# Kernel tuning notes

Hardware: AMD Instinct MI355X
Metric: run time of the kernel (lower is better)

The kernel has to match this reference:

```python
import math
import jax, jax.numpy as jnp
import numpy as np

NL, D, FF, V, S, BS, H = 6, 256, 1024, 1024, 48, 64, 8
NUM_CONT, NUM_CAT = 32, 16
TEMP = 0.1

def _pos_enc(L, d):
    pos = jnp.arange(L, dtype=jnp.float32)[:, None]
    div = jnp.exp(jnp.arange(0, d, 2, dtype=jnp.float32) * (-math.log(10000.0) / d))
    pe = jnp.zeros((L, d), jnp.float32)
    pe = pe.at[:, 0::2].set(jnp.sin(pos * div))
    pe = pe.at[:, 1::2].set(jnp.cos(pos * div))
    return pe

def _ln(x, w, b, eps=1e-5):
    m = x.mean(-1, keepdims=True)
    v = ((x - m) ** 2).mean(-1, keepdims=True)
    return (x - m) * jax.lax.rsqrt(v + eps) * w + b

def _mha(q_in, kv_in, wqkv, bqkv, wo, bo, mask=None):
    d = q_in.shape[-1]; dh = d // H
    wq, wk, wv = jnp.split(wqkv, 3, axis=0)
    bq, bk, bv = jnp.split(bqkv, 3)
    def proj(x, w, b):
        y = x @ w.T + b
        return y.reshape(x.shape[0], x.shape[1], H, dh).transpose(0, 2, 1, 3)
    q, k, v = proj(q_in, wq, bq), proj(kv_in, wk, bk), proj(kv_in, wv, bv)
    s = jnp.einsum('bhqd,bhkd->bhqk', q, k) * (1.0 / math.sqrt(dh))
    if mask is not None:
        s = s + mask
    a = jax.nn.softmax(s, axis=-1)
    o = jnp.einsum('bhqk,bhkd->bhqd', a, v).transpose(0, 2, 1, 3).reshape(q_in.shape)
    return o @ wo.T + bo

def setup_inputs() -> dict:
    key = jax.random.key(0)
    ks = iter(jax.random.split(key, 64))
    g = lambda shape: jax.random.normal(next(ks), shape, jnp.float32) * 0.02
    return dict(
        x_cont=jax.random.randint(next(ks), (BS, NUM_CONT), 0, V),
        x_cat=jax.random.randint(next(ks), (BS, NUM_CAT), 0, V),
        sos=g((1, 1, D)),
        emb_tab=g((S, V, D)),            # stacked per-feature embedding tables
        head_w=g((S, V, D)), head_b=jnp.zeros((S, V)),
        enc_wqkv=g((NL, 3 * D, D)), enc_bqkv=jnp.zeros((NL, 3 * D)),
        enc_wo=g((NL, D, D)), enc_bo=jnp.zeros((NL, D)),
        enc_w1=g((NL, FF, D)), enc_b1=jnp.zeros((NL, FF)),
        enc_w2=g((NL, D, FF)), enc_b2=jnp.zeros((NL, D)),
        enc_lnw=jnp.ones((NL, 2, D)), enc_lnb=jnp.zeros((NL, 2, D)),
        dec_swqkv=g((NL, 3 * D, D)), dec_sbqkv=jnp.zeros((NL, 3 * D)),
        dec_swo=g((NL, D, D)), dec_sbo=jnp.zeros((NL, D)),
        dec_cwqkv=g((NL, 3 * D, D)), dec_cbqkv=jnp.zeros((NL, 3 * D)),
        dec_cwo=g((NL, D, D)), dec_cbo=jnp.zeros((NL, D)),
        dec_w1=g((NL, FF, D)), dec_b1=jnp.zeros((NL, FF)),
        dec_w2=g((NL, D, FF)), dec_b2=jnp.zeros((NL, D)),
        dec_lnw=jnp.ones((NL, 3, D)), dec_lnb=jnp.zeros((NL, 3, D)),
        lnf_w=jnp.ones((2, D)), lnf_b=jnp.zeros((2, D)),
    )

def reference(x_cont, x_cat, sos, emb_tab, head_w, head_b,
              enc_wqkv, enc_bqkv, enc_wo, enc_bo, enc_w1, enc_b1, enc_w2, enc_b2,
              enc_lnw, enc_lnb,
              dec_swqkv, dec_sbqkv, dec_swo, dec_sbo,
              dec_cwqkv, dec_cbqkv, dec_cwo, dec_cbo,
              dec_w1, dec_b1, dec_w2, dec_b2, dec_lnw, dec_lnb, lnf_w, lnf_b):
    bs = x_cont.shape[0]
    pe = _pos_enc(S + 1, D)
    # ---- encoder over the 48 source features (post-norm, ReLU) ----
    idx = jnp.concatenate([x_cont, x_cat], axis=1)            # [bs, S]
    x = emb_tab[jnp.arange(S)[None, :], idx] + pe[None, :S]   # [bs, S, D]
    for l in range(NL):
        a = _mha(x, x, enc_wqkv[l], enc_bqkv[l], enc_wo[l], enc_bo[l])
        x = _ln(x + a, enc_lnw[l, 0], enc_lnb[l, 0])
        f = jax.nn.relu(x @ enc_w1[l].T + enc_b1[l]) @ enc_w2[l].T + enc_b2[l]
        x = _ln(x + f, enc_lnw[l, 1], enc_lnb[l, 1])
    memory = _ln(x, lnf_w[0], lnf_b[0])

    Lt = S + 1
    causal = jnp.triu(jnp.full((Lt, Lt), -1e9, jnp.float32), k=1)

    def decode(tgt):  # full decoder stack recomputed every step (no KV cache)
        y = tgt
        for l in range(NL):
            a = _mha(y, y, dec_swqkv[l], dec_sbqkv[l], dec_swo[l], dec_sbo[l], causal)
            y = _ln(y + a, dec_lnw[l, 0], dec_lnb[l, 0])
            c = _mha(y, memory, dec_cwqkv[l], dec_cbqkv[l], dec_cwo[l], dec_cbo[l])
            y = _ln(y + c, dec_lnw[l, 1], dec_lnb[l, 1])
            f = jax.nn.relu(y @ dec_w1[l].T + dec_b1[l]) @ dec_w2[l].T + dec_b2[l]
            y = _ln(y + f, dec_lnw[l, 2], dec_lnb[l, 2])
        return _ln(y, lnf_w[1], lnf_b[1])

    buf0 = jnp.zeros((bs, Lt, D), jnp.float32).at[:, 0].set(sos[0, 0])
    step_keys = jax.random.split(jax.random.key(42), S)

    def step(buf, xs):
        i, k, hw, hb, et = xs
        h = decode(buf + pe[None])          # [bs, Lt, D]
        hi = jnp.take(h, i, axis=1)          # last generated position [bs, D]
        logits = hi @ hw.T + hb              # [bs, V]
        choice = jax.random.categorical(k, logits / TEMP)
        buf = buf.at[:, i + 1].set(et[choice])
        return buf, (choice, logits)

    _, (choices, logits_all) = jax.lax.scan(
        step, buf0, (jnp.arange(S), step_keys, head_w, head_b, emb_tab))
    s_cont = choices[:NUM_CONT].T            # [bs, num_cont]
    s_cat = choices[NUM_CONT:].T             # [bs, num_cat]
    return s_cont, s_cat, logits_all
```

## Files before the change

kernel.cpp:

```cpp
#include <hip/hip_runtime.h>
#include <math.h>

#define JAX_PARTITIONABLE 1


static constexpr int SWQKVT  = 0;
static constexpr int SWOT    = SWQKVT + 6*256*768;
static constexpr int CWQT    = SWOT   + 6*256*256;
static constexpr int CWOT    = CWQT   + 6*256*256;
static constexpr int DW1T    = CWOT   + 6*256*256;
static constexpr int DW2T    = DW1T   + 6*256*1024;
static constexpr int WT_END  = DW2T   + 6*1024*256;
static constexpr int CKT_OFF = WT_END;
static constexpr int CV_OFF  = CKT_OFF + 6*64*48*256;
static constexpr int SKT_OFF = CV_OFF  + 6*64*48*256;
static constexpr int SV_OFF  = SKT_OFF + 6*64*48*256;
static constexpr int WS_END  = SV_OFF  + 6*64*48*256;
static constexpr int X_OFF    = 0;
static constexpr int MEM_OFF  = X_OFF + 3072*256;
static constexpr int QKV_OFF  = SKT_OFF;
static constexpr int AO_OFF   = QKV_OFF + 3072*768;
static constexpr int RES1_OFF = AO_OFF + 3072*256;
static constexpr int X1_OFF   = RES1_OFF + 3072*256;
static constexpr int HB_OFF   = SV_OFF;
static constexpr int RES2_OFF = HB_OFF + 3072*1024;
static constexpr int PCK_OFF  = SKT_OFF;

struct GParams {
  const int   *xc, *xct;
  const float *sos, *emb, *hw, *hb;
  const float *ewqkv, *ebqkv, *ewo, *ebo, *ew1, *eb1, *ew2, *eb2, *elnw, *elnb;
  const float *swqkv, *sbqkv, *swo, *sbo;
  const float *cwqkv, *cbqkv, *cwo, *cbo;
  const float *dw1, *db1, *dw2, *db2, *dlnw, *dlnb, *lnfw, *lnfb;
  float *out;
  float *ws;
};

__device__ unsigned g_cntA = 0, g_genA = 0;

static __device__ __forceinline__ void gbar(unsigned* cnt, unsigned* gen, unsigned nb) {
  __syncthreads();
  if (threadIdx.x == 0) {
    __threadfence();
    unsigned g = __hip_atomic_load(gen, __ATOMIC_RELAXED, __HIP_MEMORY_SCOPE_AGENT);
    unsigned prev = __hip_atomic_fetch_add(cnt, 1u, __ATOMIC_ACQ_REL, __HIP_MEMORY_SCOPE_AGENT);
    if (prev == nb - 1u) {
      __hip_atomic_store(cnt, 0u, __ATOMIC_RELAXED, __HIP_MEMORY_SCOPE_AGENT);
      __threadfence();
      __hip_atomic_store(gen, g + 1u, __ATOMIC_RELEASE, __HIP_MEMORY_SCOPE_AGENT);
    } else {
      while (__hip_atomic_load(gen, __ATOMIC_ACQUIRE, __HIP_MEMORY_SCOPE_AGENT) == g)
        __builtin_amdgcn_s_sleep(1);
      __threadfence();
    }
  }
  __syncthreads();
}

static __device__ __forceinline__ void tf2x32(unsigned k0, unsigned k1, unsigned& x0, unsigned& x1) {
  unsigned ks2 = k0 ^ k1 ^ 0x1BD11BDAu;
  x0 += k0; x1 += k1;
#define TF_R(r) { x0 += x1; x1 = (x1 << r) | (x1 >> (32 - r)); x1 ^= x0; }
  TF_R(13) TF_R(15) TF_R(26) TF_R(6)   x0 += k1;  x1 += ks2 + 1u;
  TF_R(17) TF_R(29) TF_R(16) TF_R(24)  x0 += ks2; x1 += k0  + 2u;
  TF_R(13) TF_R(15) TF_R(26) TF_R(6)   x0 += k0;  x1 += k1  + 3u;
  TF_R(17) TF_R(29) TF_R(16) TF_R(24)  x0 += k1;  x1 += ks2 + 4u;
  TF_R(13) TF_R(15) TF_R(26) TF_R(6)   x0 += ks2; x1 += k0  + 5u;
#undef TF_R
}

static __device__ __forceinline__ void step_key(int i, unsigned& k0, unsigned& k1) {
#if JAX_PARTITIONABLE
  unsigned x0 = 0u, x1 = (unsigned)i;
  tf2x32(0u, 42u, x0, x1);
  k0 = x0; k1 = x1;
#else
  unsigned w[2];
  for (int wi = 0; wi < 2; wi++) {
    unsigned o = (unsigned)(2*i + wi), x0, x1;
    if (o < 48u) { x0 = o; x1 = 48u + o; tf2x32(0u, 42u, x0, x1); w[wi] = x0; }
    else         { x0 = o - 48u; x1 = o; tf2x32(0u, 42u, x0, x1); w[wi] = x1; }
  }
  k0 = w[0]; k1 = w[1];
#endif
}

static __device__ __forceinline__ unsigned gumbel_bits(unsigned k0, unsigned k1, int b, int v) {
#if JAX_PARTITIONABLE
  unsigned x0 = 0u, x1 = (unsigned)(b*1024 + v);
  tf2x32(k0, k1, x0, x1);
  return x0 ^ x1;
#else
  unsigned jj = (unsigned)((b & 31)*1024 + v);
  unsigned x0 = jj, x1 = 32768u + jj;
  tf2x32(k0, k1, x0, x1);
  return (b < 32) ? x0 : x1;
#endif
}

static __device__ __forceinline__ float pe_val(int p, int c) {
  const float KC = (float)(-9.210340371976184 / 256.0);
  int j = c >> 1;
  float dv = expf((float)(2*j) * KC);
  float a = (float)p * dv;
  return (c & 1) ? cosf(a) : sinf(a);
}

static __device__ __forceinline__ void wave_ln_row(float* row, const float* lw, const float* lb) {
  const int lane = threadIdx.x & 63;
  float x0 = row[lane], x1 = row[lane+64], x2 = row[lane+128], x3 = row[lane+192];
  float s = (x0 + x1) + (x2 + x3);
#pragma unroll
  for (int m = 1; m < 64; m <<= 1) s += __shfl_xor(s, m);
  float mean = s * 0.00390625f;
  float d0 = x0-mean, d1 = x1-mean, d2 = x2-mean, d3 = x3-mean;
  float q = (d0*d0 + d1*d1) + (d2*d2 + d3*d3);
#pragma unroll
  for (int m = 1; m < 64; m <<= 1) q += __shfl_xor(q, m);
  float rs = 1.0f / sqrtf(q * 0.00390625f + 1e-5f);
  row[lane]     = d0*rs*lw[lane]     + lb[lane];
  row[lane+64]  = d1*rs*lw[lane+64]  + lb[lane+64];
  row[lane+128] = d2*rs*lw[lane+128] + lb[lane+128];
  row[lane+192] = d3*rs*lw[lane+192] + lb[lane+192];
}

template<int C, int KS, int K>
static __device__ void matvec_t(const float* __restrict__ wt, const float* __restrict__ x,
                                float* __restrict__ part) {
  const int t = threadIdx.x;
  constexpr int O4 = C/4;
  constexpr int KC = K/KS;
  if (t < O4*KS) {
    const int kc = t / O4, o4 = t - kc*O4;
    const int k0 = kc*KC;
    float4 acc = {0.f,0.f,0.f,0.f};
    const float* wp = wt + k0*C + o4*4;
    for (int kb = 0; kb < KC; kb += 16) {
      float4 w[16];
#pragma unroll
      for (int j = 0; j < 16; j++) w[j] = *(const float4*)(wp + (kb + j)*C);
#pragma unroll
      for (int j4 = 0; j4 < 4; j4++) {
        float4 xv = *(const float4*)(x + k0 + kb + j4*4);
        float4 a0 = w[j4*4+0], a1 = w[j4*4+1], a2 = w[j4*4+2], a3 = w[j4*4+3];
        acc.x += xv.x*a0.x; acc.y += xv.x*a0.y; acc.z += xv.x*a0.z; acc.w += xv.x*a0.w;
        acc.x += xv.y*a1.x; acc.y += xv.y*a1.y; acc.z += xv.y*a1.z; acc.w += xv.y*a1.w;
        acc.x += xv.z*a2.x; acc.y += xv.z*a2.y; acc.z += xv.z*a2.z; acc.w += xv.z*a2.w;
        acc.x += xv.w*a3.x; acc.y += xv.w*a3.y; acc.z += xv.w*a3.z; acc.w += xv.w*a3.w;
      }
    }
    *(float4*)(part + kc*C + o4*4) = acc;
  }
  __syncthreads();
}

static __device__ void gemm_stage(const float* __restrict__ A, const float* __restrict__ W,
                                  const float* __restrict__ bias, const float* __restrict__ res,
                                  float* __restrict__ out, int R, int C, int K, int relu,
                                  float* sA) {
  const int t = threadIdx.x;
  const bool act = (t < 256);
  const int lane = t & 63, wv = (t >> 6) & 3;
  const int ntc = C >> 6;
  const int ntiles = (R >> 5) * ntc;
  for (int tile = blockIdx.x; tile < ntiles; tile += gridDim.x) {
    const int tr = tile / ntc, tc = tile - tr*ntc;
    const int r0 = tr << 5;
    const int c  = (tc << 6) + lane;
    float acc[8] = {0,0,0,0,0,0,0,0};
    for (int kc = 0; kc < K; kc += 256) {
      __syncthreads();
      if (act) {
#pragma unroll
        for (int u = 0; u < 8; u++) {
          int idx = u*256 + t;
          int rr = idx >> 6, cc = idx & 63;
          ((float4*)sA)[idx] = *(const float4*)(A + (r0+rr)*K + kc + cc*4);
        }
      }
      __syncthreads();
      if (act) {
        const float* wr = W + c*K + kc;
        for (int k = 0; k < 256; k += 4) {
          float4 w4 = *(const float4*)(wr + k);
#pragma unroll
          for (int r = 0; r < 8; r++) {
            float4 a4 = *(const float4*)(sA + (wv*8 + r)*256 + k);
            acc[r] += a4.x*w4.x; acc[r] += a4.y*w4.y; acc[r] += a4.z*w4.z; acc[r] += a4.w*w4.w;
          }
        }
      }
    }
    if (act) {
      float bb = bias ? bias[c] : 0.0f;
#pragma unroll
      for (int r = 0; r < 8; r++) {
        int row = r0 + wv*8 + r;
        float v = acc[r] + bb;
        if (relu) v = fmaxf(v, 0.0f);
        if (res)  v += res[row*C + c];
        out[row*C + c] = v;
      }
    }
  }
}

static __device__ void ln_stage(const float* in, const float* lw, const float* lb,
                                float* out, int R) {
  const int lane = threadIdx.x & 63;
  int gw = blockIdx.x*8 + (threadIdx.x >> 6);
  for (int row = gw; row < R; row += gridDim.x*8) {
    const float* ir = in + row*256;
    float x0 = ir[lane], x1 = ir[lane+64], x2 = ir[lane+128], x3 = ir[lane+192];
    float s = (x0 + x1) + (x2 + x3);
#pragma unroll
    for (int m = 1; m < 64; m <<= 1) s += __shfl_xor(s, m);
    float mean = s * 0.00390625f;
    float d0 = x0-mean, d1 = x1-mean, d2 = x2-mean, d3 = x3-mean;
    float q = (d0*d0 + d1*d1) + (d2*d2 + d3*d3);
#pragma unroll
    for (int m = 1; m < 64; m <<= 1) q += __shfl_xor(q, m);
    float rs = 1.0f / sqrtf(q * 0.00390625f + 1e-5f);
    float* orow = out + row*256;
    orow[lane]     = d0*rs*lw[lane]     + lb[lane];
    orow[lane+64]  = d1*rs*lw[lane+64]  + lb[lane+64];
    orow[lane+128] = d2*rs*lw[lane+128] + lb[lane+128];
    orow[lane+192] = d3*rs*lw[lane+192] + lb[lane+192];
  }
}

static __device__ void attn_core(const float* qd, const float* kb, const float* vb,
                                 int krstride, int kstride, int nk,
                                 float* sc, float* red, float* ao) {
  const int t = threadIdx.x;
  const int r = t >> 5, p0 = t & 31;
  const bool act = (t < 256);
  if (act) {
#pragma unroll
    for (int pass = 0; pass < 2; pass++) {
      int p = pass*32 + p0;
      if (p < nk) {
        const float4* k4 = (const float4*)(kb + r*krstride + p*kstride);
        const float4* q4 = (const float4*)(qd + r*32);
        float a = 0.0f;
#pragma unroll
        for (int d4 = 0; d4 < 8; d4++) {
          float4 kv = k4[d4], qv = q4[d4];
          a += qv.x*kv.x; a += qv.y*kv.y; a += qv.z*kv.z; a += qv.w*kv.w;
        }
        sc[r*48 + p] = a * 0.17677669529663687f;
      }
    }
  }
  __syncthreads();
  if (t < 8) {
    float m = sc[t*48];
    for (int p = 1; p < nk; p++) m = fmaxf(m, sc[t*48 + p]);
    red[t] = m;
  }
  __syncthreads();
  if (act) {
#pragma unroll
    for (int pass = 0; pass < 2; pass++) {
      int p = pass*32 + p0;
      if (p < nk) sc[r*48 + p] = expf(sc[r*48 + p] - red[r]);
    }
  }
  __syncthreads();
  if (t < 8) {
    float s = 0.0f;
    for (int p = 0; p < nk; p++) s += sc[t*48 + p];
    red[8 + t] = s;
  }
  __syncthreads();
  if (act) {
#pragma unroll
    for (int pass = 0; pass < 2; pass++) {
      int p = pass*32 + p0;
      if (p < nk) sc[r*48 + p] = sc[r*48 + p] / red[8 + r];
    }
  }
  __syncthreads();
  if (act) {
    const int d2 = t & 31;
    const float* vr = vb + r*krstride + d2;
    float a = 0.0f;
    for (int p = 0; p < nk; p++) a += sc[r*48 + p] * vr[p*kstride];
    ao[r*32 + d2] = a;
  }
  __syncthreads();
}

static __device__ void enc_attn_stage(const float* QKV, float* AO, float* sm) {
  const int t = threadIdx.x;
  const bool act = (t < 256);
  float* qd  = sm;
  float* sc  = sm + 256;
  float* ao  = sm + 640;
  float* red = sm + 896;
  for (int pi = blockIdx.x; pi < 512; pi += gridDim.x) {
    int b = pi >> 3, h = pi & 7;
    const float* Qb = QKV + b*48*768 + h*32;
    const float* Kb = QKV + b*48*768 + 256 + h*32;
    const float* Vb = QKV + b*48*768 + 512 + h*32;
    for (int qg = 0; qg < 6; qg++) {
      if (act) { int r = t >> 5, d2 = t & 31; qd[r*32 + d2] = Qb[(qg*8 + r)*768 + d2]; }
      __syncthreads();
      attn_core(qd, Kb, Vb, 0, 768, 48, sc, red, ao);
      if (act) { int r = t >> 5, d2 = t & 31; AO[(b*48 + qg*8 + r)*256 + h*32 + d2] = ao[r*32 + d2]; }
      __syncthreads();
    }
  }
}

static __device__ void attn_dec(const float* qd, const float* kt, const float* v,
                                int nk, float* sc, float* red, float* ao) {
  const int t = threadIdx.x;
  const int r = t >> 5, p0 = t & 31;
  const bool act = (t < 256);
  if (act) {
    const float4* q4 = (const float4*)(qd + r*32);
#pragma unroll
    for (int pass = 0; pass < 2; pass++) {
      int p = pass*32 + p0;
      if (p < nk) {
        const float* kb = kt + r*1536 + p*4;
        float a = 0.0f;
#pragma unroll
        for (int j = 0; j < 8; j++) {
          float4 kv = *(const float4*)(kb + j*192);
          float4 qv = q4[j];
          a += qv.x*kv.x; a += qv.y*kv.y; a += qv.z*kv.z; a += qv.w*kv.w;
        }
        sc[r*48 + p] = a * 0.17677669529663687f;
      }
    }
  }
  __syncthreads();
  if (t < 8) {
    float m = sc[t*48];
    for (int p = 1; p < nk; p++) m = fmaxf(m, sc[t*48 + p]);
    red[t] = m;
  }
  __syncthreads();
  if (act) {
#pragma unroll
    for (int pass = 0; pass < 2; pass++) {
      int p = pass*32 + p0;
      if (p < nk) sc[r*48 + p] = expf(sc[r*48 + p] - red[r]);
    }
  }
  __syncthreads();
  if (t < 8) {
    float s = 0.0f;
    for (int p = 0; p < nk; p++) s += sc[t*48 + p];
    red[8 + t] = s;
  }
  __syncthreads();
  if (act) {
#pragma unroll
    for (int pass = 0; pass < 2; pass++) {
      int p = pass*32 + p0;
      if (p < nk) sc[r*48 + p] = sc[r*48 + p] / red[8 + r];
    }
  }
  __syncthreads();
  if (act) {
    const int d2 = t & 31;
    const float* vr = v + r*32 + d2;
    float a = 0.0f;
    int p = 0;
    for (; p + 8 <= nk; p += 8) {
      float vv[8], ss[8];
#pragma unroll
      for (int j = 0; j < 8; j++) { vv[j] = vr[(p+j)*256]; ss[j] = sc[r*48 + p + j]; }
#pragma unroll
      for (int j = 0; j < 8; j++) a += ss[j] * vv[j];
    }
    for (; p < nk; p++) a += sc[r*48 + p] * vr[p*256];
    ao[r*32 + d2] = a;
  }
  __syncthreads();
}

__global__ void __launch_bounds__(512)
genrev5_kernel(GParams P) {
  __shared__ float sm[8448];
  float* ws = P.ws;
  const int wg = blockIdx.x;
  const int t  = threadIdx.x;

  if (t < 256) {
    for (int rr = 0; rr < 12; rr++) {
      int row = wg*12 + rr;
      int b = row / 48, s = row % 48;
      int tok = (s < 32) ? P.xc[b*32 + s] : P.xct[b*16 + (s - 32)];
      ws[X_OFF + row*256 + t] = P.emb[(s*1024 + tok)*256 + t] + pe_val(s, t);
    }
  }
  gbar(&g_cntA, &g_genA, 256);

  float* Xp = ws + X_OFF;
  for (int l = 0; l < 6; l++) {
    gemm_stage(Xp, P.ewqkv + l*768*256, P.ebqkv + l*768, nullptr, ws + QKV_OFF, 3072, 768, 256, 0, sm);
    gbar(&g_cntA, &g_genA, 256);
    enc_attn_stage(ws + QKV_OFF, ws + AO_OFF, sm);
    gbar(&g_cntA, &g_genA, 256);
    gemm_stage(ws + AO_OFF, P.ewo + l*256*256, P.ebo + l*256, Xp, ws + RES1_OFF, 3072, 256, 256, 0, sm);
    gbar(&g_cntA, &g_genA, 256);
    ln_stage(ws + RES1_OFF, P.elnw + (l*2 + 0)*256, P.elnb + (l*2 + 0)*256, ws + X1_OFF, 3072);
    gbar(&g_cntA, &g_genA, 256);
    gemm_stage(ws + X1_OFF, P.ew1 + l*1024*256, P.eb1 + l*1024, nullptr, ws + HB_OFF, 3072, 1024, 256, 1, sm);
    gbar(&g_cntA, &g_genA, 256);
    gemm_stage(ws + HB_OFF, P.ew2 + l*256*1024, P.eb2 + l*256, ws + X1_OFF, ws + RES2_OFF, 3072, 256, 1024, 0, sm);
    gbar(&g_cntA, &g_genA, 256);
    ln_stage(ws + RES2_OFF, P.elnw + (l*2 + 1)*256, P.elnb + (l*2 + 1)*256, Xp, 3072);
    gbar(&g_cntA, &g_genA, 256);
  }
  ln_stage(Xp, P.lnfw, P.lnfb, ws + MEM_OFF, 3072);
  gbar(&g_cntA, &g_genA, 256);
  for (int l = 0; l < 6; l++) {
    gemm_stage(ws + MEM_OFF, P.cwqkv + (l*768 + 256)*256, P.cbqkv + l*768 + 256, nullptr,
               ws + PCK_OFF + l*786432, 3072, 256, 256, 0, sm);
    gemm_stage(ws + MEM_OFF, P.cwqkv + (l*768 + 512)*256, P.cbqkv + l*768 + 512, nullptr,
               ws + CV_OFF + l*786432, 3072, 256, 256, 0, sm);
  }
  gbar(&g_cntA, &g_genA, 256);

  {
    const int gt = wg*512 + t;
    const int GT = 256*512;
    for (int idx = gt; idx < 6*256*768; idx += GT) {
      int l = idx / 196608, r = idx - l*196608;
      int k = r / 768, o = r - k*768;
      ws[SWQKVT + idx] = P.swqkv[(l*768 + o)*256 + k];
    }
    for (int idx = gt; idx < 6*65536; idx += GT) {
      int l = idx >> 16, r = idx & 65535, k = r >> 8, o = r & 255;
      ws[SWOT + idx] = P.swo[(l*256 + o)*256 + k];
    }
    for (int idx = gt; idx < 6*65536; idx += GT) {
      int l = idx >> 16, r = idx & 65535, k = r >> 8, o = r & 255;
      ws[CWQT + idx] = P.cwqkv[(l*768 + o)*256 + k];
    }
    for (int idx = gt; idx < 6*65536; idx += GT) {
      int l = idx >> 16, r = idx & 65535, k = r >> 8, o = r & 255;
      ws[CWOT + idx] = P.cwo[(l*256 + o)*256 + k];
    }
    for (int idx = gt; idx < 6*262144; idx += GT) {
      int l = idx >> 18, r = idx & 262143, k = r >> 10, o = r & 1023;
      ws[DW1T + idx] = P.dw1[(l*1024 + o)*256 + k];
    }
    for (int idx = gt; idx < 6*262144; idx += GT) {
      int l = idx >> 18, r = idx & 262143, k = r >> 8, o = r & 255;
      ws[DW2T + idx] = P.dw2[(l*256 + o)*1024 + k];
    }
    for (int idx = gt; idx < 6*64*48*256; idx += GT) {
      int l = idx / 786432, r = idx - l*786432;
      int b = r / 12288, q = r - b*12288;
      int d4 = q / 192, s2 = q - d4*192;
      int p = s2 >> 2, c = s2 & 3;
      ws[CKT_OFF + idx] = ws[PCK_OFF + l*786432 + (b*48 + p)*256 + d4*4 + c];
    }
  }
  gbar(&g_cntA, &g_genA, 256);

  if (wg >= 64) return;
  const int b = wg;

  float* cur  = sm;
  float* qv   = sm + 256;
  float* av   = sm + 512;
  float* y1   = sm + 768;
  float* y2   = sm + 1024;
  float* hbf  = sm + 1280;
  float* sc   = sm + 2304;
  float* red  = sm + 2688;
  float* y0   = sm + 2720;
  float* bvv  = sm + 2976;
  int*   bii  = (int*)(sm + 3232);
  float* part = sm + 3488;

  if (t < 256) y0[t] = P.sos[t] + pe_val(0, t);
  __syncthreads();

  for (int i = 0; i < 48; i++) {
    if (t < 256) cur[t] = y0[t];
    __syncthreads();
    for (int l = 0; l < 6; l++) {
      const int skt = SKT_OFF + l*786432 + b*12288;
      const int sv  = SV_OFF  + l*786432 + b*12288;
      const int ckt = CKT_OFF + l*786432 + b*12288;
      const int cv  = CV_OFF  + l*786432 + b*12288;
      matvec_t<768,2,256>(ws + SWQKVT + l*196608, cur, part);
      for (int o = t; o < 768; o += 512) {
        float v = part[o] + part[768 + o] + P.sbqkv[l*768 + o];
        if (o < 256)      qv[o] = v;
        else if (o < 512) { int d = o - 256; ws[skt + (d>>2)*192 + i*4 + (d&3)] = v; }
        else              ws[sv + i*256 + (o - 512)] = v;
      }
      __syncthreads();
      attn_dec(qv, ws + skt, ws + sv, i + 1, sc, red, av);
      matvec_t<256,8,256>(ws + SWOT + l*65536, av, part);
      if (t < 256) {
        float s = part[t];
#pragma unroll
        for (int kc = 1; kc < 8; kc++) s += part[kc*256 + t];
        y1[t] = cur[t] + (s + P.sbo[l*256 + t]);
      }
      __syncthreads();
      if (t < 64) wave_ln_row(y1, P.dlnw + (l*3 + 0)*256, P.dlnb + (l*3 + 0)*256);
      __syncthreads();
      matvec_t<256,8,256>(ws + CWQT + l*65536, y1, part);
      if (t < 256) {
        float s = part[t];
#pragma unroll
        for (int kc = 1; kc < 8; kc++) s += part[kc*256 + t];
        qv[t] = s + P.cbqkv[l*768 + t];
      }
      __syncthreads();
      attn_dec(qv, ws + ckt, ws + cv, 48, sc, red, av);
      matvec_t<256,8,256>(ws + CWOT + l*65536, av, part);
      if (t < 256) {
        float s = part[t];
#pragma unroll
        for (int kc = 1; kc < 8; kc++) s += part[kc*256 + t];
        y2[t] = y1[t] + (s + P.cbo[l*256 + t]);
      }
      __syncthreads();
      if (t < 64) wave_ln_row(y2, P.dlnw + (l*3 + 1)*256, P.dlnb + (l*3 + 1)*256);
      __syncthreads();
      matvec_t<1024,2,256>(ws + DW1T + l*262144, y2, part);
      for (int o = t; o < 1024; o += 512)
        hbf[o] = fmaxf(part[o] + part[1024 + o] + P.db1[l*1024 + o], 0.0f);
      __syncthreads();
      matvec_t<256,8,1024>(ws + DW2T + l*262144, hbf, part);
      if (t < 256) {
        float s = part[t];
#pragma unroll
        for (int kc = 1; kc < 8; kc++) s += part[kc*256 + t];
        cur[t] = y2[t] + (s + P.db2[l*256 + t]);
      }
      __syncthreads();
      if (t < 64) wave_ln_row(cur, P.dlnw + (l*3 + 2)*256, P.dlnb + (l*3 + 2)*256);
      __syncthreads();
    }
    if (t < 64) wave_ln_row(cur, P.lnfw + 256, P.lnfb + 256);
    __syncthreads();
    {
      const int wv = t >> 6, lane = t & 63;
      const float4 x4 = *(const float4*)(cur + lane*4);
      for (int base = 0; base < 1024; base += 16) {
        int o = base + wv, o2 = o + 8;
        float4 wa = *(const float4*)(P.hw + (size_t)(i*1024 + o)*256 + lane*4);
        float4 wb = *(const float4*)(P.hw + (size_t)(i*1024 + o2)*256 + lane*4);
        float sa = wa.x*x4.x; sa += wa.y*x4.y; sa += wa.z*x4.z; sa += wa.w*x4.w;
        float sb = wb.x*x4.x; sb += wb.y*x4.y; sb += wb.z*x4.z; sb += wb.w*x4.w;
#pragma unroll
        for (int m = 1; m < 64; m <<= 1) { sa += __shfl_xor(sa, m); sb += __shfl_xor(sb, m); }
        if (lane == 0) {
          hbf[o]  = sa + P.hb[i*1024 + o];
          hbf[o2] = sb + P.hb[i*1024 + o2];
        }
      }
    }
    __syncthreads();
    for (int o = t; o < 1024; o += 512)
      P.out[3072 + i*65536 + b*1024 + o] = hbf[o];
    __syncthreads();
    unsigned k0, k1;
    step_key(i, k0, k1);
    if (t < 256) {
      float bestv = -INFINITY; int besti = 0;
#pragma unroll
      for (int e = 0; e < 4; e++) {
        int v = t*4 + e;
        unsigned bits = gumbel_bits(k0, k1, b, v);
        float f = __uint_as_float((bits >> 9) | 0x3f800000u);
        float u = fmaxf(f - 1.0f, 1.17549435e-38f);
        float g = -logf(-logf(u));
        float z = g + hbf[v] / 0.1f;
        if (z > bestv) { bestv = z; besti = v; }
      }
      bvv[t] = bestv; bii[t] = besti;
    }
    __syncthreads();
    for (int s = 128; s > 0; s >>= 1) {
      if (t < s) {
        float ov = bvv[t+s]; int oi = bii[t+s];
        if (ov > bvv[t] || (ov == bvv[t] && oi < bii[t])) { bvv[t] = ov; bii[t] = oi; }
      }
      __syncthreads();
    }
    const int ch = bii[0];
    if (t == 0) {
      if (i < 32) P.out[b*32 + i] = (float)ch;
      else        P.out[2048 + b*16 + (i - 32)] = (float)ch;
    }
    if (t < 256) y0[t] = P.emb[(i*1024 + ch)*256 + t] + pe_val(i + 1, t);
    __syncthreads();
  }
}

extern "C" void kernel_launch(void* const* d_in, const int* in_sizes, int n_in,
                              void* d_out, int out_size, void* d_ws, size_t ws_size,
                              hipStream_t stream) {
  (void)in_sizes; (void)n_in; (void)out_size; (void)ws_size;
  GParams p;
  p.xc    = (const int*)  d_in[0];
  p.xct   = (const int*)  d_in[1];
  p.sos   = (const float*)d_in[2];
  p.emb   = (const float*)d_in[3];
  p.hw    = (const float*)d_in[4];
  p.hb    = (const float*)d_in[5];
  p.ewqkv = (const float*)d_in[6];
  p.ebqkv = (const float*)d_in[7];
  p.ewo   = (const float*)d_in[8];
  p.ebo   = (const float*)d_in[9];
  p.ew1   = (const float*)d_in[10];
  p.eb1   = (const float*)d_in[11];
  p.ew2   = (const float*)d_in[12];
  p.eb2   = (const float*)d_in[13];
  p.elnw  = (const float*)d_in[14];
  p.elnb  = (const float*)d_in[15];
  p.swqkv = (const float*)d_in[16];
  p.sbqkv = (const float*)d_in[17];
  p.swo   = (const float*)d_in[18];
  p.sbo   = (const float*)d_in[19];
  p.cwqkv = (const float*)d_in[20];
  p.cbqkv = (const float*)d_in[21];
  p.cwo   = (const float*)d_in[22];
  p.cbo   = (const float*)d_in[23];
  p.dw1   = (const float*)d_in[24];
  p.db1   = (const float*)d_in[25];
  p.dw2   = (const float*)d_in[26];
  p.db2   = (const float*)d_in[27];
  p.dlnw  = (const float*)d_in[28];
  p.dlnb  = (const float*)d_in[29];
  p.lnfw  = (const float*)d_in[30];
  p.lnfb  = (const float*)d_in[31];
  p.out   = (float*)d_out;
  p.ws    = (float*)d_ws;
  hipLaunchKernelGGL(genrev5_kernel, dim3(256), dim3(512), 0, stream, p);
}
```

Before: 23.42 ms.

## Add soft cohort syncs for decode blocks, widen matvec batches, unroll reductions

Adds a soft, bounded-spin cohort sync among groups of 8 decode blocks before each layer and before the output head. The aim is to keep blocks that read the same weights in rough lockstep so those weight reads are shared through cache. Separately, the matvec weight prefetch batch grows from 16 to 32 rows, the softmax max/sum loops are unrolled by 8, and the head logits loop gets unroll 4. The sync counters live in newly used workspace past the old end, which requires a large enough workspace allocation, and the spin-waits can add latency.

```diff
diff --git a/kernel.cpp b/kernel.cpp
--- a/kernel.cpp
+++ b/kernel.cpp
@@ -25,6 +25,7 @@
 static constexpr int HB_OFF   = SV_OFF;
 static constexpr int RES2_OFF = HB_OFF + 3072*1024;
 static constexpr int PCK_OFF  = SKT_OFF;
+static constexpr int SSYNC_OFF = WS_END;
 
 struct GParams {
   const int   *xc, *xct;
@@ -58,6 +59,18 @@
   __syncthreads();
 }
 
+static __device__ __forceinline__ void cohort_sync(unsigned* slot) {
+  __syncthreads();
+  if (threadIdx.x == 0) {
+    __hip_atomic_fetch_add(slot, 1u, __ATOMIC_RELAXED, __HIP_MEMORY_SCOPE_AGENT);
+    for (int it = 0; it < 64; ++it) {
+      if (__hip_atomic_load(slot, __ATOMIC_RELAXED, __HIP_MEMORY_SCOPE_AGENT) >= 8u) break;
+      __builtin_amdgcn_s_sleep(1);
+    }
+  }
+  __syncthreads();
+}
+
 static __device__ __forceinline__ void tf2x32(unsigned k0, unsigned k1, unsigned& x0, unsigned& x1) {
   unsigned ks2 = k0 ^ k1 ^ 0x1BD11BDAu;
   x0 += k0; x1 += k1;
@@ -131,17 +144,18 @@
   const int t = threadIdx.x;
   constexpr int O4 = C/4;
   constexpr int KC = K/KS;
+  constexpr int BT = (KC < 32) ? KC : 32;
   if (t < O4*KS) {
     const int kc = t / O4, o4 = t - kc*O4;
     const int k0 = kc*KC;
     float4 acc = {0.f,0.f,0.f,0.f};
     const float* wp = wt + k0*C + o4*4;
-    for (int kb = 0; kb < KC; kb += 16) {
-      float4 w[16];
-#pragma unroll
-      for (int j = 0; j < 16; j++) w[j] = *(const float4*)(wp + (kb + j)*C);
-#pragma unroll
-      for (int j4 = 0; j4 < 4; j4++) {
+    for (int kb = 0; kb < KC; kb += BT) {
+      float4 w[BT];
+#pragma unroll
+      for (int j = 0; j < BT; j++) w[j] = *(const float4*)(wp + (kb + j)*C);
+#pragma unroll
+      for (int j4 = 0; j4 < BT/4; j4++) {
         float4 xv = *(const float4*)(x + k0 + kb + j4*4);
         float4 a0 = w[j4*4+0], a1 = w[j4*4+1], a2 = w[j4*4+2], a3 = w[j4*4+3];
         acc.x += xv.x*a0.x; acc.y += xv.x*a0.y; acc.z += xv.x*a0.z; acc.w += xv.x*a0.w;
@@ -339,8 +353,16 @@
   }
   __syncthreads();
   if (t < 8) {
-    float m = sc[t*48];
-    for (int p = 1; p < nk; p++) m = fmaxf(m, sc[t*48 + p]);
+    const float* scr = sc + t*48;
+    float m = scr[0];
+    int p = 1;
+    for (; p + 8 <= nk; p += 8) {
+      float s0=scr[p],s1=scr[p+1],s2=scr[p+2],s3=scr[p+3],
+            s4=scr[p+4],s5=scr[p+5],s6=scr[p+6],s7=scr[p+7];
+      m=fmaxf(m,s0); m=fmaxf(m,s1); m=fmaxf(m,s2); m=fmaxf(m,s3);
+      m=fmaxf(m,s4); m=fmaxf(m,s5); m=fmaxf(m,s6); m=fmaxf(m,s7);
+    }
+    for (; p < nk; p++) m = fmaxf(m, scr[p]);
     red[t] = m;
   }
   __syncthreads();
@@ -353,8 +375,15 @@
   }
   __syncthreads();
   if (t < 8) {
+    const float* scr = sc + t*48;
     float s = 0.0f;
-    for (int p = 0; p < nk; p++) s += sc[t*48 + p];
+    int p = 0;
+    for (; p + 8 <= nk; p += 8) {
+      float s0=scr[p],s1=scr[p+1],s2=scr[p+2],s3=scr[p+3],
+            s4=scr[p+4],s5=scr[p+5],s6=scr[p+6],s7=scr[p+7];
+      s+=s0; s+=s1; s+=s2; s+=s3; s+=s4; s+=s5; s+=s6; s+=s7;
+    }
+    for (; p < nk; p++) s += scr[p];
     red[8 + t] = s;
   }
   __syncthreads();
@@ -385,7 +414,7 @@
 }
 
 __global__ void __launch_bounds__(512)
-genrev5_kernel(GParams P) {
+genrev6_kernel(GParams P) {
   __shared__ float sm[8448];
   float* ws = P.ws;
   const int wg = blockIdx.x;
@@ -463,11 +492,16 @@
       int p = s2 >> 2, c = s2 & 3;
       ws[CKT_OFF + idx] = ws[PCK_OFF + l*786432 + (b*48 + p)*256 + d4*4 + c];
     }
+    unsigned* ssync = (unsigned*)(ws + SSYNC_OFF);
+    for (int idx = gt; idx < 3072; idx += GT)
+      __hip_atomic_store(&ssync[idx], 0u, __ATOMIC_RELAXED, __HIP_MEMORY_SCOPE_AGENT);
   }
   gbar(&g_cntA, &g_genA, 256);
 
   if (wg >= 64) return;
   const int b = wg;
+  const int grp = wg & 7;
+  unsigned* ssync = (unsigned*)(ws + SSYNC_OFF);
 
   float* cur  = sm;
   float* qv   = sm + 256;
@@ -489,6 +523,7 @@
     if (t < 256) cur[t] = y0[t];
     __syncthreads();
     for (int l = 0; l < 6; l++) {
+      cohort_sync(ssync + (i*7 + l)*8 + grp);
       const int skt = SKT_OFF + l*786432 + b*12288;
       const int sv  = SV_OFF  + l*786432 + b*12288;
       const int ckt = CKT_OFF + l*786432 + b*12288;
@@ -548,9 +583,11 @@
     }
     if (t < 64) wave_ln_row(cur, P.lnfw + 256, P.lnfb + 256);
     __syncthreads();
+    cohort_sync(ssync + (i*7 + 6)*8 + grp);
     {
       const int wv = t >> 6, lane = t & 63;
       const float4 x4 = *(const float4*)(cur + lane*4);
+#pragma unroll 4
       for (int base = 0; base < 1024; base += 16) {
         int o = base + wv, o2 = o + 8;
         float4 wa = *(const float4*)(P.hw + (size_t)(i*1024 + o)*256 + lane*4);
@@ -642,5 +679,5 @@
   p.lnfb  = (const float*)d_in[31];
   p.out   = (float*)d_out;
   p.ws    = (float*)d_ws;
-  hipLaunchKernelGGL(genrev5_kernel, dim3(256), dim3(512), 0, stream, p);
-}
+  hipLaunchKernelGGL(genrev6_kernel, dim3(256), dim3(512), 0, stream, p);
+}
```

New measurement: 23.00 ms. Within noise of the previous version (-1.8%).
